# Performance work log

Measured on AMD Instinct MI355X. Metric: run time of the kernel, lower is better.

The kernel has to match this reference:

```python
import jax, jax.numpy as jnp
import numpy as np

N_USERS = 100_000
N_ITEMS = 50_000
N_EDGES = 2_000_000
D = 64
ALPHA = 0.5      # tanh-blend coefficient (alpha)
NORM_2 = -1.0    # exponent on back-aggregation degree norm (args.norm_2)


def setup_inputs() -> dict:
    key = jax.random.key(0)
    k1, k2, k3, k4, k5 = jax.random.split(key, 5)
    return {
        "h_user": jax.random.normal(k1, (N_USERS, D), jnp.float32) * 0.1,
        "pretrained_feature": jax.random.normal(k2, (N_ITEMS, D), jnp.float32),
        "edge_w": jax.random.normal(k3, (N_ITEMS, 1), jnp.float32),
        "src_idx": jax.random.randint(k4, (N_EDGES,), 0, N_USERS, dtype=jnp.int32),
        "dst_idx": jax.random.randint(k5, (N_EDGES,), 0, N_ITEMS, dtype=jnp.int32),
    }


def reference(h_user, pretrained_feature, edge_w, src_idx, dst_idx):
    # HGCNLayer.forward: bidirectional copy_src+sum aggregation with degree norm,
    # tanh prompt blend and node-softmax edge weighting.
    ones = jnp.ones((N_EDGES,), h_user.dtype)

    # forward pass user -> item: rst[d] = sum_{(s,d) in E} h_user[s]
    rst = jax.ops.segment_sum(h_user[src_idx], dst_idx, num_segments=N_ITEMS)  # [N_ITEMS, D]
    deg_dst = jnp.clip(jax.ops.segment_sum(ones, dst_idx, num_segments=N_ITEMS), 1.0)

    # alpha * tanh prompt blend
    rst = rst + ALPHA * jnp.tanh(pretrained_feature)
    # edge-prompt softmax scaling (softmax over nodes; see notes)
    rst = jax.nn.softmax(edge_w, axis=0) * rst
    # in-degree^-1 normalization
    rst = rst / deg_dst[:, None]

    # backward pass item -> user: bsrc[s] = sum_{(s,d) in E} rst[d]
    bsrc = jax.ops.segment_sum(rst[dst_idx], src_idx, num_segments=N_USERS)  # [N_USERS, D]
    deg_src = jnp.clip(jax.ops.segment_sum(ones, src_idx, num_segments=N_USERS), 1.0)
    bsrc = bsrc * jnp.power(deg_src, NORM_2)[:, None]
    return bsrc
```

## Files before the change

### kernel.cpp

```cpp
#include <hip/hip_runtime.h>
#include <hip/hip_bf16.h>
#include <math.h>

#define N_USERS 100000
#define N_ITEMS 50000
#define N_EDGES 2000000
#define D 64

#define FB_BINS 98
#define BB_BINS 196
#define NBINS   (FB_BINS + BB_BINS)
#define CHUNK   2048
#define NCHUNK  ((N_EDGES + CHUNK - 1) / CHUNK)
#define FOFF_F_N (FB_BINS * 512 + 1)
#define FOFF_B_N (BB_BINS * 512 + 1)
#define TOTSLOT  (2 * N_EDGES)
#define FWD_WGS (N_ITEMS / 16)
#define BWD_WGS ((N_USERS + 15) / 16)

__device__ __forceinline__ float blo(unsigned u) {
    union { unsigned i; float f; } c; c.i = u << 16; return c.f;
}
__device__ __forceinline__ float bhi(unsigned u) {
    union { unsigned i; float f; } c; c.i = u & 0xFFFF0000u; return c.f;
}
__device__ __forceinline__ unsigned bpack(float x, float y) {
    __hip_bfloat16 a = __float2bfloat16(x), b = __float2bfloat16(y);
    unsigned short ua = *reinterpret_cast<unsigned short*>(&a);
    unsigned short ub = *reinterpret_cast<unsigned short*>(&b);
    return (unsigned)ua | ((unsigned)ub << 16);
}

__global__ __launch_bounds__(256) void prep_kernel(
    const float2* __restrict__ hin, unsigned* __restrict__ hu16,
    const int* __restrict__ src, const int* __restrict__ dst,
    int* __restrict__ gh) {
    __shared__ int h[NBINS];
    for (int i = threadIdx.x; i < NBINS; i += 256) h[i] = 0;
    __syncthreads();
    int stride = gridDim.x * blockDim.x;
    int t0 = blockIdx.x * blockDim.x + threadIdx.x;
    for (int i = t0; i < N_USERS * 32; i += stride) {
        float2 v = hin[i];
        hu16[i] = bpack(v.x, v.y);
    }
    for (int e = t0; e < N_EDGES; e += stride) {
        atomicAdd(&h[dst[e] >> 9], 1);
        atomicAdd(&h[FB_BINS + (src[e] >> 9)], 1);
    }
    __syncthreads();
    for (int i = threadIdx.x; i < NBINS; i += 256) {
        int v = h[i];
        if (v) atomicAdd(&gh[i], v);
    }
}

__global__ void scan_soft_kernel(const int* __restrict__ in, int* __restrict__ out,
                                 int* __restrict__ cur,
                                 const float* __restrict__ w, float* __restrict__ stats) {
    __shared__ float redf[16];
    __shared__ int wsum[16];
    int tid = threadIdx.x, lane = tid & 63, wid = tid >> 6;

    if (blockIdx.x == 0) {
        int idx0 = tid * 4;
        int v[4]; int tot = 0;
#pragma unroll
        for (int e = 0; e < 4; e++) {
            int i = idx0 + e;
            v[e] = (i < NBINS) ? in[i] : 0;
            tot += v[e];
        }
        int incl = tot;
#pragma unroll
        for (int off = 1; off < 64; off <<= 1) {
            int t = __shfl_up(incl, off);
            if (lane >= off) incl += t;
        }
        if (lane == 63) wsum[wid] = incl;
        __syncthreads();
        if (wid == 0 && lane < 16) {
            int t = wsum[lane];
            int sc = t;
#pragma unroll
            for (int off = 1; off < 16; off <<= 1) {
                int u = __shfl_up(sc, off);
                if (lane >= off) sc += u;
            }
            wsum[lane] = sc - t;
        }
        __syncthreads();
        int excl = wsum[wid] + incl - tot;
#pragma unroll
        for (int e = 0; e < 4; e++) {
            int i = idx0 + e;
            if (i < NBINS) { out[i] = excl; cur[i] = excl; }
            if (i == NBINS) out[i] = excl;
            excl += v[e];
        }
        if (tid == 1023) out[NBINS] = excl;
        return;
    }

    float m = -INFINITY;
    for (int i = tid; i < N_ITEMS; i += 1024) m = fmaxf(m, w[i]);
#pragma unroll
    for (int off = 32; off; off >>= 1) m = fmaxf(m, __shfl_xor(m, off));
    if (lane == 0) redf[wid] = m;
    __syncthreads();
    if (tid == 0) {
        float t = redf[0];
        for (int k = 1; k < 16; k++) t = fmaxf(t, redf[k]);
        redf[0] = t;
    }
    __syncthreads();
    m = redf[0];
    __syncthreads();

    float s = 0.f;
    for (int i = tid; i < N_ITEMS; i += 1024) s += expf(w[i] - m);
#pragma unroll
    for (int off = 32; off; off >>= 1) s += __shfl_xor(s, off);
    if (lane == 0) redf[wid] = s;
    __syncthreads();
    if (tid == 0) {
        float t = 0.f;
        for (int k = 0; k < 16; k++) t += redf[k];
        stats[0] = m;
        stats[1] = t;
    }
}

__global__ __launch_bounds__(256) void binfill_kernel(
    const int* __restrict__ src, const int* __restrict__ dst,
    int* __restrict__ gcur, unsigned* __restrict__ stage) {
    __shared__ int cnt[NBINS];
    __shared__ int gbase[NBINS];
    __shared__ int lcur[NBINS];
    int c = blockIdx.x;
    int base = c * CHUNK;
    int nEdge = N_EDGES - base; if (nEdge > CHUNK) nEdge = CHUNK;

    for (int t = threadIdx.x; t < NBINS; t += 256) { cnt[t] = 0; lcur[t] = 0; }
    __syncthreads();

    int es[8], ed[8];
#pragma unroll
    for (int j = 0; j < 8; j++) {
        int k = j * 256 + threadIdx.x;
        if (k < nEdge) {
            es[j] = src[base + k];
            ed[j] = dst[base + k];
            atomicAdd(&cnt[ed[j] >> 9], 1);
            atomicAdd(&cnt[FB_BINS + (es[j] >> 9)], 1);
        } else {
            es[j] = -1;
        }
    }
    __syncthreads();
    for (int t = threadIdx.x; t < NBINS; t += 256) {
        int cv = cnt[t];
        gbase[t] = cv ? atomicAdd(&gcur[t], cv) : 0;
    }
    __syncthreads();
#pragma unroll
    for (int j = 0; j < 8; j++) {
        if (es[j] >= 0) {
            int s = es[j], d = ed[j];
            int bf = d >> 9;
            int p = atomicAdd(&lcur[bf], 1);
            stage[gbase[bf] + p] = (unsigned)s | ((unsigned)(d & 511) << 17);
            int bb = FB_BINS + (s >> 9);
            int q = atomicAdd(&lcur[bb], 1);
            stage[gbase[bb] + q] = (unsigned)d | ((unsigned)(s & 511) << 16);
        }
    }
}

__global__ __launch_bounds__(512) void redist3_kernel(
    const unsigned* __restrict__ stage, const int* __restrict__ binoff,
    unsigned* __restrict__ stage2, int* __restrict__ foff_f, int* __restrict__ foff_b) {
    __shared__ int cnt[512];
    __shared__ int wsum[8];
    int wg = blockIdx.x, t = threadIdx.x, lane = t & 63, wv = t >> 6;

    if (wg < FB_BINS) {
        int B = wg;
        int beg = binoff[B], end = binoff[B + 1];
        cnt[t] = 0;
        __syncthreads();
        for (int k = beg + t; k < end; k += 512) {
            unsigned e = stage[k];
            atomicAdd(&cnt[(e >> 17) & 511], 1);
        }
        __syncthreads();
        int v = cnt[t];
        int incl = v;
#pragma unroll
        for (int off = 1; off < 64; off <<= 1) {
            int u = __shfl_up(incl, off);
            if (lane >= off) incl += u;
        }
        if (lane == 63) wsum[wv] = incl;
        __syncthreads();
        if (t == 0) {
            int run = 0;
#pragma unroll
            for (int k2 = 0; k2 < 8; k2++) { int x = wsum[k2]; wsum[k2] = run; run += x; }
        }
        __syncthreads();
        int base = beg + wsum[wv] + incl - v;
        foff_f[(B << 9) | t] = base;
        cnt[t] = base;
        if (B == FB_BINS - 1 && t == 0) foff_f[FB_BINS * 512] = end;
        __syncthreads();
        for (int k = beg + t; k < end; k += 512) {
            unsigned e = stage[k];
            int p = atomicAdd(&cnt[(e >> 17) & 511], 1);
            stage2[p] = e & 0x1FFFFu;
        }
    } else {
        for (int pass = 0; pass < 2; pass++) {
            int B = FB_BINS + ((wg - FB_BINS) << 1) + pass;
            int beg = binoff[B], end = binoff[B + 1];
            cnt[t] = 0;
            __syncthreads();
            for (int k = beg + t; k < end; k += 512) {
                unsigned e = stage[k];
                atomicAdd(&cnt[(e >> 16) & 511], 1);
            }
            __syncthreads();
            int v = cnt[t];
            int incl = v;
#pragma unroll
            for (int off = 1; off < 64; off <<= 1) {
                int u = __shfl_up(incl, off);
                if (lane >= off) incl += u;
            }
            if (lane == 63) wsum[wv] = incl;
            __syncthreads();
            if (t == 0) {
                int run = 0;
#pragma unroll
                for (int k2 = 0; k2 < 8; k2++) { int x = wsum[k2]; wsum[k2] = run; run += x; }
            }
            __syncthreads();
            int base = beg + wsum[wv] + incl - v;
            foff_b[((B - FB_BINS) << 9) | t] = base;
            cnt[t] = base;
            if (B == NBINS - 1 && t == 0) foff_b[BB_BINS * 512] = end;
            __syncthreads();
            for (int k = beg + t; k < end; k += 512) {
                unsigned e = stage[k];
                int p = atomicAdd(&cnt[(e >> 16) & 511], 1);
                stage2[p] = e & 0xFFFFu;
            }
            __syncthreads();
        }
    }
}

__global__ __launch_bounds__(256) void fwd_gather_kernel(
    const unsigned* __restrict__ hu16, const float* __restrict__ pf,
    const float* __restrict__ edge_w, const unsigned* __restrict__ stage2,
    const int* __restrict__ foff_f, const float* __restrict__ stats,
    unsigned* __restrict__ rst16) {
    int tid = threadIdx.x, lane = tid & 63, wv = tid >> 6;
    int q = lane & 31, half = lane >> 5;
    float m = stats[0], ssum = stats[1];
    const float2* PF2 = (const float2*)pf;
    int i0 = blockIdx.x * 16;

    for (int il = wv; il < 16; il += 4) {
        int i = i0 + il;
        if (i >= N_ITEMS) break;
        int a = foff_f[i], b = foff_f[i + 1];
        float ax = 0.f, ay = 0.f;
        int k = a;
        for (; k + 16 <= b; k += 16) {
            int s0 = (int)__builtin_nontemporal_load(&stage2[k + half]);
            int s1 = (int)__builtin_nontemporal_load(&stage2[k + 2 + half]);
            int s2 = (int)__builtin_nontemporal_load(&stage2[k + 4 + half]);
            int s3 = (int)__builtin_nontemporal_load(&stage2[k + 6 + half]);
            int s4 = (int)__builtin_nontemporal_load(&stage2[k + 8 + half]);
            int s5 = (int)__builtin_nontemporal_load(&stage2[k + 10 + half]);
            int s6 = (int)__builtin_nontemporal_load(&stage2[k + 12 + half]);
            int s7 = (int)__builtin_nontemporal_load(&stage2[k + 14 + half]);
            unsigned u0 = hu16[(s0 << 5) + q];
            unsigned u1 = hu16[(s1 << 5) + q];
            unsigned u2 = hu16[(s2 << 5) + q];
            unsigned u3 = hu16[(s3 << 5) + q];
            unsigned u4 = hu16[(s4 << 5) + q];
            unsigned u5 = hu16[(s5 << 5) + q];
            unsigned u6 = hu16[(s6 << 5) + q];
            unsigned u7 = hu16[(s7 << 5) + q];
            ax += ((blo(u0) + blo(u1)) + (blo(u2) + blo(u3)))
                + ((blo(u4) + blo(u5)) + (blo(u6) + blo(u7)));
            ay += ((bhi(u0) + bhi(u1)) + (bhi(u2) + bhi(u3)))
                + ((bhi(u4) + bhi(u5)) + (bhi(u6) + bhi(u7)));
        }
        if (k + 8 <= b) {
            int s0 = (int)__builtin_nontemporal_load(&stage2[k + half]);
            int s1 = (int)__builtin_nontemporal_load(&stage2[k + 2 + half]);
            int s2 = (int)__builtin_nontemporal_load(&stage2[k + 4 + half]);
            int s3 = (int)__builtin_nontemporal_load(&stage2[k + 6 + half]);
            unsigned u0 = hu16[(s0 << 5) + q];
            unsigned u1 = hu16[(s1 << 5) + q];
            unsigned u2 = hu16[(s2 << 5) + q];
            unsigned u3 = hu16[(s3 << 5) + q];
            ax += (blo(u0) + blo(u1)) + (blo(u2) + blo(u3));
            ay += (bhi(u0) + bhi(u1)) + (bhi(u2) + bhi(u3));
            k += 8;
        }
        for (; k + 2 <= b; k += 2) {
            unsigned u = hu16[((int)__builtin_nontemporal_load(&stage2[k + half]) << 5) + q];
            ax += blo(u); ay += bhi(u);
        }
        if (k < b && half == 0) {
            unsigned u = hu16[((int)__builtin_nontemporal_load(&stage2[k]) << 5) + q];
            ax += blo(u); ay += bhi(u);
        }
        ax += __shfl_xor(ax, 32);
        ay += __shfl_xor(ay, 32);
        if (half == 0) {
            float deg = (float)(b - a);
            if (deg < 1.f) deg = 1.f;
            float sc = expf(edge_w[i] - m) / (ssum * deg);
            float2 pv = PF2[(size_t)i * 32 + q];
            float vx = (ax + 0.5f * tanhf(pv.x)) * sc;
            float vy = (ay + 0.5f * tanhf(pv.y)) * sc;
            rst16[(size_t)i * 32 + q] = bpack(vx, vy);
        }
    }
}

__global__ __launch_bounds__(256) void bwd_gather_kernel(
    const unsigned* __restrict__ rst16, const unsigned* __restrict__ stage2,
    const int* __restrict__ foff_b, float* __restrict__ out) {
    int tid = threadIdx.x, lane = tid & 63, wv = tid >> 6;
    int q = lane & 31, half = lane >> 5;
    float2* OUT2 = (float2*)out;
    int u0i = blockIdx.x * 16;

    for (int il = wv; il < 16; il += 4) {
        int u = u0i + il;
        if (u >= N_USERS) break;
        int a = foff_b[u], b = foff_b[u + 1];
        float ax = 0.f, ay = 0.f;
        int k = a;
        for (; k + 16 <= b; k += 16) {
            int d0 = (int)__builtin_nontemporal_load(&stage2[k + half]);
            int d1 = (int)__builtin_nontemporal_load(&stage2[k + 2 + half]);
            int d2 = (int)__builtin_nontemporal_load(&stage2[k + 4 + half]);
            int d3 = (int)__builtin_nontemporal_load(&stage2[k + 6 + half]);
            int d4 = (int)__builtin_nontemporal_load(&stage2[k + 8 + half]);
            int d5 = (int)__builtin_nontemporal_load(&stage2[k + 10 + half]);
            int d6 = (int)__builtin_nontemporal_load(&stage2[k + 12 + half]);
            int d7 = (int)__builtin_nontemporal_load(&stage2[k + 14 + half]);
            unsigned u0 = rst16[(d0 << 5) + q];
            unsigned u1 = rst16[(d1 << 5) + q];
            unsigned u2 = rst16[(d2 << 5) + q];
            unsigned u3 = rst16[(d3 << 5) + q];
            unsigned u4 = rst16[(d4 << 5) + q];
            unsigned u5 = rst16[(d5 << 5) + q];
            unsigned u6 = rst16[(d6 << 5) + q];
            unsigned u7 = rst16[(d7 << 5) + q];
            ax += ((blo(u0) + blo(u1)) + (blo(u2) + blo(u3)))
                + ((blo(u4) + blo(u5)) + (blo(u6) + blo(u7)));
            ay += ((bhi(u0) + bhi(u1)) + (bhi(u2) + bhi(u3)))
                + ((bhi(u4) + bhi(u5)) + (bhi(u6) + bhi(u7)));
        }
        if (k + 8 <= b) {
            int d0 = (int)__builtin_nontemporal_load(&stage2[k + half]);
            int d1 = (int)__builtin_nontemporal_load(&stage2[k + 2 + half]);
            int d2 = (int)__builtin_nontemporal_load(&stage2[k + 4 + half]);
            int d3 = (int)__builtin_nontemporal_load(&stage2[k + 6 + half]);
            unsigned u0 = rst16[(d0 << 5) + q];
            unsigned u1 = rst16[(d1 << 5) + q];
            unsigned u2 = rst16[(d2 << 5) + q];
            unsigned u3 = rst16[(d3 << 5) + q];
            ax += (blo(u0) + blo(u1)) + (blo(u2) + blo(u3));
            ay += (bhi(u0) + bhi(u1)) + (bhi(u2) + bhi(u3));
            k += 8;
        }
        for (; k + 2 <= b; k += 2) {
            unsigned e = rst16[((int)__builtin_nontemporal_load(&stage2[k + half]) << 5) + q];
            ax += blo(e); ay += bhi(e);
        }
        if (k < b && half == 0) {
            unsigned e = rst16[((int)__builtin_nontemporal_load(&stage2[k]) << 5) + q];
            ax += blo(e); ay += bhi(e);
        }
        ax += __shfl_xor(ax, 32);
        ay += __shfl_xor(ay, 32);
        if (half == 0) {
            float deg = (float)(b - a);
            if (deg < 1.f) deg = 1.f;
            OUT2[(size_t)u * 32 + q] = make_float2(ax / deg, ay / deg);
        }
    }
}

extern "C" void kernel_launch(void* const* d_in, const int* in_sizes, int n_in,
                              void* d_out, int out_size, void* d_ws, size_t ws_size,
                              hipStream_t stream) {
    const float* h_user = (const float*)d_in[0];
    const float* pf     = (const float*)d_in[1];
    const float* edge_w = (const float*)d_in[2];
    const int*   src    = (const int*)d_in[3];
    const int*   dst    = (const int*)d_in[4];
    float* out = (float*)d_out;

    char* p = (char*)d_ws;
    int* gh      = (int*)p;     p += sizeof(int) * NBINS;
    int* binoff  = (int*)p;     p += sizeof(int) * (NBINS + 1);
    int* gcur    = (int*)p;     p += sizeof(int) * NBINS;
    int* foff_f  = (int*)p;     p += sizeof(int) * FOFF_F_N;
    int* foff_b  = (int*)p;     p += sizeof(int) * FOFF_B_N;
    float* stats = (float*)p;   p += 4 * sizeof(float);
    unsigned* stage  = (unsigned*)p; p += sizeof(unsigned) * (size_t)TOTSLOT;
    unsigned* stage2 = (unsigned*)p; p += sizeof(unsigned) * (size_t)TOTSLOT;
    unsigned* hu16   = (unsigned*)p; p += sizeof(unsigned) * (size_t)N_USERS * 32;
    unsigned* rst16  = (unsigned*)p; p += sizeof(unsigned) * (size_t)N_ITEMS * 32;

    hipMemsetAsync(gh, 0, sizeof(int) * NBINS, stream);

    prep_kernel<<<1024, 256, 0, stream>>>((const float2*)h_user, hu16, src, dst, gh);
    scan_soft_kernel<<<2, 1024, 0, stream>>>(gh, binoff, gcur, edge_w, stats);
    binfill_kernel<<<NCHUNK, 256, 0, stream>>>(src, dst, gcur, stage);
    redist3_kernel<<<196, 512, 0, stream>>>(stage, binoff, stage2, foff_f, foff_b);
    fwd_gather_kernel<<<FWD_WGS, 256, 0, stream>>>(hu16, pf, edge_w, stage2, foff_f, stats, rst16);
    bwd_gather_kernel<<<BWD_WGS, 256, 0, stream>>>(rst16, stage2, foff_b, out);
}
```

Measured before the change: 344.3 us.

## Shard forward gather by source range to improve cache locality

```diff
diff --git a/kernel.cpp b/kernel.cpp
--- a/kernel.cpp
+++ b/kernel.cpp
@@ -10,13 +10,14 @@
 #define FB_BINS 98
 #define BB_BINS 196
 #define NBINS   (FB_BINS + BB_BINS)
-#define CHUNK   2048
+#define CHUNK   4096
 #define NCHUNK  ((N_EDGES + CHUNK - 1) / CHUNK)
-#define FOFF_F_N (FB_BINS * 512 + 1)
+#define FOFF_F_N (FB_BINS * 1024 + 1)
 #define FOFF_B_N (BB_BINS * 512 + 1)
 #define TOTSLOT  (2 * N_EDGES)
 #define FWD_WGS (N_ITEMS / 16)
 #define BWD_WGS ((N_USERS + 15) / 16)
+#define SHARD_SPLIT 50000
 
 __device__ __forceinline__ float blo(unsigned u) {
     union { unsigned i; float f; } c; c.i = u << 16; return c.f;
@@ -29,6 +30,55 @@
     unsigned short ua = *reinterpret_cast<unsigned short*>(&a);
     unsigned short ub = *reinterpret_cast<unsigned short*>(&b);
     return (unsigned)ua | ((unsigned)ub << 16);
+}
+
+__device__ __forceinline__ void gather_run(
+    const unsigned* __restrict__ tbl, const unsigned* __restrict__ stage2,
+    int a, int b, int q, int half, float& ax, float& ay) {
+    int k = a;
+    for (; k + 16 <= b; k += 16) {
+        int s0 = (int)__builtin_nontemporal_load(&stage2[k + half]);
+        int s1 = (int)__builtin_nontemporal_load(&stage2[k + 2 + half]);
+        int s2 = (int)__builtin_nontemporal_load(&stage2[k + 4 + half]);
+        int s3 = (int)__builtin_nontemporal_load(&stage2[k + 6 + half]);
+        int s4 = (int)__builtin_nontemporal_load(&stage2[k + 8 + half]);
+        int s5 = (int)__builtin_nontemporal_load(&stage2[k + 10 + half]);
+        int s6 = (int)__builtin_nontemporal_load(&stage2[k + 12 + half]);
+        int s7 = (int)__builtin_nontemporal_load(&stage2[k + 14 + half]);
+        unsigned u0 = tbl[(s0 << 5) + q];
+        unsigned u1 = tbl[(s1 << 5) + q];
+        unsigned u2 = tbl[(s2 << 5) + q];
+        unsigned u3 = tbl[(s3 << 5) + q];
+        unsigned u4 = tbl[(s4 << 5) + q];
+        unsigned u5 = tbl[(s5 << 5) + q];
+        unsigned u6 = tbl[(s6 << 5) + q];
+        unsigned u7 = tbl[(s7 << 5) + q];
+        ax += ((blo(u0) + blo(u1)) + (blo(u2) + blo(u3)))
+            + ((blo(u4) + blo(u5)) + (blo(u6) + blo(u7)));
+        ay += ((bhi(u0) + bhi(u1)) + (bhi(u2) + bhi(u3)))
+            + ((bhi(u4) + bhi(u5)) + (bhi(u6) + bhi(u7)));
+    }
+    if (k + 8 <= b) {
+        int s0 = (int)__builtin_nontemporal_load(&stage2[k + half]);
+        int s1 = (int)__builtin_nontemporal_load(&stage2[k + 2 + half]);
+        int s2 = (int)__builtin_nontemporal_load(&stage2[k + 4 + half]);
+        int s3 = (int)__builtin_nontemporal_load(&stage2[k + 6 + half]);
+        unsigned u0 = tbl[(s0 << 5) + q];
+        unsigned u1 = tbl[(s1 << 5) + q];
+        unsigned u2 = tbl[(s2 << 5) + q];
+        unsigned u3 = tbl[(s3 << 5) + q];
+        ax += (blo(u0) + blo(u1)) + (blo(u2) + blo(u3));
+        ay += (bhi(u0) + bhi(u1)) + (bhi(u2) + bhi(u3));
+        k += 8;
+    }
+    for (; k + 2 <= b; k += 2) {
+        unsigned u = tbl[((int)__builtin_nontemporal_load(&stage2[k + half]) << 5) + q];
+        ax += blo(u); ay += bhi(u);
+    }
+    if (k < b && half == 0) {
+        unsigned u = tbl[((int)__builtin_nontemporal_load(&stage2[k]) << 5) + q];
+        ax += blo(u); ay += bhi(u);
+    }
 }
 
 __global__ __launch_bounds__(256) void prep_kernel(
@@ -98,7 +148,6 @@
             if (i == NBINS) out[i] = excl;
             excl += v[e];
         }
-        if (tid == 1023) out[NBINS] = excl;
         return;
     }
 
@@ -144,9 +193,9 @@
     for (int t = threadIdx.x; t < NBINS; t += 256) { cnt[t] = 0; lcur[t] = 0; }
     __syncthreads();
 
-    int es[8], ed[8];
-#pragma unroll
-    for (int j = 0; j < 8; j++) {
+    int es[16], ed[16];
+#pragma unroll
+    for (int j = 0; j < 16; j++) {
         int k = j * 256 + threadIdx.x;
         if (k < nEdge) {
             es[j] = src[base + k];
@@ -164,7 +213,7 @@
     }
     __syncthreads();
 #pragma unroll
-    for (int j = 0; j < 8; j++) {
+    for (int j = 0; j < 16; j++) {
         if (es[j] >= 0) {
             int s = es[j], d = ed[j];
             int bf = d >> 9;
@@ -180,21 +229,24 @@
 __global__ __launch_bounds__(512) void redist3_kernel(
     const unsigned* __restrict__ stage, const int* __restrict__ binoff,
     unsigned* __restrict__ stage2, int* __restrict__ foff_f, int* __restrict__ foff_b) {
-    __shared__ int cnt[512];
+    __shared__ int cnt[1024];
     __shared__ int wsum[8];
     int wg = blockIdx.x, t = threadIdx.x, lane = t & 63, wv = t >> 6;
 
     if (wg < FB_BINS) {
         int B = wg;
         int beg = binoff[B], end = binoff[B + 1];
-        cnt[t] = 0;
+        cnt[t] = 0; cnt[t + 512] = 0;
         __syncthreads();
         for (int k = beg + t; k < end; k += 512) {
             unsigned e = stage[k];
-            atomicAdd(&cnt[(e >> 17) & 511], 1);
-        }
-        __syncthreads();
-        int v = cnt[t];
+            int key = (int)((e >> 17) & 511) << 1;
+            key |= ((e & 0x1FFFFu) >= SHARD_SPLIT) ? 1 : 0;
+            atomicAdd(&cnt[key], 1);
+        }
+        __syncthreads();
+        int c0 = cnt[t << 1], c1 = cnt[(t << 1) | 1];
+        int v = c0 + c1;
         int incl = v;
 #pragma unroll
         for (int off = 1; off < 64; off <<= 1) {
@@ -210,13 +262,18 @@
         }
         __syncthreads();
         int base = beg + wsum[wv] + incl - v;
-        foff_f[(B << 9) | t] = base;
-        cnt[t] = base;
-        if (B == FB_BINS - 1 && t == 0) foff_f[FB_BINS * 512] = end;
+        int slot = (B << 10) | (t << 1);
+        foff_f[slot] = base;
+        foff_f[slot | 1] = base + c0;
+        cnt[t << 1] = base;
+        cnt[(t << 1) | 1] = base + c0;
+        if (B == FB_BINS - 1 && t == 0) foff_f[FB_BINS * 1024] = end;
         __syncthreads();
         for (int k = beg + t; k < end; k += 512) {
             unsigned e = stage[k];
-            int p = atomicAdd(&cnt[(e >> 17) & 511], 1);
+            int key = (int)((e >> 17) & 511) << 1;
+            key |= ((e & 0x1FFFFu) >= SHARD_SPLIT) ? 1 : 0;
+            int p = atomicAdd(&cnt[key], 1);
             stage2[p] = e & 0x1FFFFu;
         }
     } else {
@@ -260,11 +317,34 @@
     }
 }
 
-__global__ __launch_bounds__(256) void fwd_gather_kernel(
+__global__ __launch_bounds__(256) void fwd_s0_kernel(
+    const unsigned* __restrict__ hu16, const unsigned* __restrict__ stage2,
+    const int* __restrict__ foff_f, float* __restrict__ pacc) {
+    int tid = threadIdx.x, lane = tid & 63, wv = tid >> 6;
+    int q = lane & 31, half = lane >> 5;
+    int i0 = blockIdx.x * 16;
+
+    for (int il = wv; il < 16; il += 4) {
+        int i = i0 + il;
+        if (i >= N_ITEMS) break;
+        int a = foff_f[i << 1], b = foff_f[(i << 1) | 1];
+        float ax = 0.f, ay = 0.f;
+        gather_run(hu16, stage2, a, b, q, half, ax, ay);
+        ax += __shfl_xor(ax, 32);
+        ay += __shfl_xor(ay, 32);
+        if (half == 0) {
+            size_t off = ((size_t)i * 32 + q) * 2;
+            __builtin_nontemporal_store(ax, &pacc[off]);
+            __builtin_nontemporal_store(ay, &pacc[off + 1]);
+        }
+    }
+}
+
+__global__ __launch_bounds__(256) void fwd_s1_kernel(
     const unsigned* __restrict__ hu16, const float* __restrict__ pf,
     const float* __restrict__ edge_w, const unsigned* __restrict__ stage2,
     const int* __restrict__ foff_f, const float* __restrict__ stats,
-    unsigned* __restrict__ rst16) {
+    const float* __restrict__ pacc, unsigned* __restrict__ rst16) {
     int tid = threadIdx.x, lane = tid & 63, wv = tid >> 6;
     int q = lane & 31, half = lane >> 5;
     float m = stats[0], ssum = stats[1];
@@ -274,56 +354,18 @@
     for (int il = wv; il < 16; il += 4) {
         int i = i0 + il;
         if (i >= N_ITEMS) break;
-        int a = foff_f[i], b = foff_f[i + 1];
+        int a = foff_f[(i << 1) | 1], b = foff_f[(i << 1) + 2];
+        int a0 = foff_f[i << 1];
         float ax = 0.f, ay = 0.f;
-        int k = a;
-        for (; k + 16 <= b; k += 16) {
-            int s0 = (int)__builtin_nontemporal_load(&stage2[k + half]);
-            int s1 = (int)__builtin_nontemporal_load(&stage2[k + 2 + half]);
-            int s2 = (int)__builtin_nontemporal_load(&stage2[k + 4 + half]);
-            int s3 = (int)__builtin_nontemporal_load(&stage2[k + 6 + half]);
-            int s4 = (int)__builtin_nontemporal_load(&stage2[k + 8 + half]);
-            int s5 = (int)__builtin_nontemporal_load(&stage2[k + 10 + half]);
-            int s6 = (int)__builtin_nontemporal_load(&stage2[k + 12 + half]);
-            int s7 = (int)__builtin_nontemporal_load(&stage2[k + 14 + half]);
-            unsigned u0 = hu16[(s0 << 5) + q];
-            unsigned u1 = hu16[(s1 << 5) + q];
-            unsigned u2 = hu16[(s2 << 5) + q];
-            unsigned u3 = hu16[(s3 << 5) + q];
-            unsigned u4 = hu16[(s4 << 5) + q];
-            unsigned u5 = hu16[(s5 << 5) + q];
-            unsigned u6 = hu16[(s6 << 5) + q];
-            unsigned u7 = hu16[(s7 << 5) + q];
-            ax += ((blo(u0) + blo(u1)) + (blo(u2) + blo(u3)))
-                + ((blo(u4) + blo(u5)) + (blo(u6) + blo(u7)));
-            ay += ((bhi(u0) + bhi(u1)) + (bhi(u2) + bhi(u3)))
-                + ((bhi(u4) + bhi(u5)) + (bhi(u6) + bhi(u7)));
-        }
-        if (k + 8 <= b) {
-            int s0 = (int)__builtin_nontemporal_load(&stage2[k + half]);
-            int s1 = (int)__builtin_nontemporal_load(&stage2[k + 2 + half]);
-            int s2 = (int)__builtin_nontemporal_load(&stage2[k + 4 + half]);
-            int s3 = (int)__builtin_nontemporal_load(&stage2[k + 6 + half]);
-            unsigned u0 = hu16[(s0 << 5) + q];
-            unsigned u1 = hu16[(s1 << 5) + q];
-            unsigned u2 = hu16[(s2 << 5) + q];
-            unsigned u3 = hu16[(s3 << 5) + q];
-            ax += (blo(u0) + blo(u1)) + (blo(u2) + blo(u3));
-            ay += (bhi(u0) + bhi(u1)) + (bhi(u2) + bhi(u3));
-            k += 8;
-        }
-        for (; k + 2 <= b; k += 2) {
-            unsigned u = hu16[((int)__builtin_nontemporal_load(&stage2[k + half]) << 5) + q];
-            ax += blo(u); ay += bhi(u);
-        }
-        if (k < b && half == 0) {
-            unsigned u = hu16[((int)__builtin_nontemporal_load(&stage2[k]) << 5) + q];
-            ax += blo(u); ay += bhi(u);
-        }
+        gather_run(hu16, stage2, a, b, q, half, ax, ay);
         ax += __shfl_xor(ax, 32);
         ay += __shfl_xor(ay, 32);
         if (half == 0) {
-            float deg = (float)(b - a);
+            size_t off = ((size_t)i * 32 + q) * 2;
+            float px = __builtin_nontemporal_load(&pacc[off]);
+            float py = __builtin_nontemporal_load(&pacc[off + 1]);
+            ax += px; ay += py;
+            float deg = (float)(b - a0);
             if (deg < 1.f) deg = 1.f;
             float sc = expf(edge_w[i] - m) / (ssum * deg);
             float2 pv = PF2[(size_t)i * 32 + q];
@@ -347,50 +389,7 @@
         if (u >= N_USERS) break;
         int a = foff_b[u], b = foff_b[u + 1];
         float ax = 0.f, ay = 0.f;
-        int k = a;
-        for (; k + 16 <= b; k += 16) {
-            int d0 = (int)__builtin_nontemporal_load(&stage2[k + half]);
-            int d1 = (int)__builtin_nontemporal_load(&stage2[k + 2 + half]);
-            int d2 = (int)__builtin_nontemporal_load(&stage2[k + 4 + half]);
-            int d3 = (int)__builtin_nontemporal_load(&stage2[k + 6 + half]);
-            int d4 = (int)__builtin_nontemporal_load(&stage2[k + 8 + half]);
-            int d5 = (int)__builtin_nontemporal_load(&stage2[k + 10 + half]);
-            int d6 = (int)__builtin_nontemporal_load(&stage2[k + 12 + half]);
-            int d7 = (int)__builtin_nontemporal_load(&stage2[k + 14 + half]);
-            unsigned u0 = rst16[(d0 << 5) + q];
-            unsigned u1 = rst16[(d1 << 5) + q];
-            unsigned u2 = rst16[(d2 << 5) + q];
-            unsigned u3 = rst16[(d3 << 5) + q];
-            unsigned u4 = rst16[(d4 << 5) + q];
-            unsigned u5 = rst16[(d5 << 5) + q];
-            unsigned u6 = rst16[(d6 << 5) + q];
-            unsigned u7 = rst16[(d7 << 5) + q];
-            ax += ((blo(u0) + blo(u1)) + (blo(u2) + blo(u3)))
-                + ((blo(u4) + blo(u5)) + (blo(u6) + blo(u7)));
-            ay += ((bhi(u0) + bhi(u1)) + (bhi(u2) + bhi(u3)))
-                + ((bhi(u4) + bhi(u5)) + (bhi(u6) + bhi(u7)));
-        }
-        if (k + 8 <= b) {
-            int d0 = (int)__builtin_nontemporal_load(&stage2[k + half]);
-            int d1 = (int)__builtin_nontemporal_load(&stage2[k + 2 + half]);
-            int d2 = (int)__builtin_nontemporal_load(&stage2[k + 4 + half]);
-            int d3 = (int)__builtin_nontemporal_load(&stage2[k + 6 + half]);
-            unsigned u0 = rst16[(d0 << 5) + q];
-            unsigned u1 = rst16[(d1 << 5) + q];
-            unsigned u2 = rst16[(d2 << 5) + q];
-            unsigned u3 = rst16[(d3 << 5) + q];
-            ax += (blo(u0) + blo(u1)) + (blo(u2) + blo(u3));
-            ay += (bhi(u0) + bhi(u1)) + (bhi(u2) + bhi(u3));
-            k += 8;
-        }
-        for (; k + 2 <= b; k += 2) {
-            unsigned e = rst16[((int)__builtin_nontemporal_load(&stage2[k + half]) << 5) + q];
-            ax += blo(e); ay += bhi(e);
-        }
-        if (k < b && half == 0) {
-            unsigned e = rst16[((int)__builtin_nontemporal_load(&stage2[k]) << 5) + q];
-            ax += blo(e); ay += bhi(e);
-        }
+        gather_run(rst16, stage2, a, b, q, half, ax, ay);
         ax += __shfl_xor(ax, 32);
         ay += __shfl_xor(ay, 32);
         if (half == 0) {
@@ -422,6 +421,7 @@
     unsigned* stage2 = (unsigned*)p; p += sizeof(unsigned) * (size_t)TOTSLOT;
     unsigned* hu16   = (unsigned*)p; p += sizeof(unsigned) * (size_t)N_USERS * 32;
     unsigned* rst16  = (unsigned*)p; p += sizeof(unsigned) * (size_t)N_ITEMS * 32;
+    float* pacc      = (float*)p;    p += sizeof(float) * (size_t)N_ITEMS * 64;
 
     hipMemsetAsync(gh, 0, sizeof(int) * NBINS, stream);
 
@@ -429,6 +429,7 @@
     scan_soft_kernel<<<2, 1024, 0, stream>>>(gh, binoff, gcur, edge_w, stats);
     binfill_kernel<<<NCHUNK, 256, 0, stream>>>(src, dst, gcur, stage);
     redist3_kernel<<<196, 512, 0, stream>>>(stage, binoff, stage2, foff_f, foff_b);
-    fwd_gather_kernel<<<FWD_WGS, 256, 0, stream>>>(hu16, pf, edge_w, stage2, foff_f, stats, rst16);
+    fwd_s0_kernel<<<FWD_WGS, 256, 0, stream>>>(hu16, stage2, foff_f, pacc);
+    fwd_s1_kernel<<<FWD_WGS, 256, 0, stream>>>(hu16, pf, edge_w, stage2, foff_f, stats, pacc, rst16);
     bwd_gather_kernel<<<BWD_WGS, 256, 0, stream>>>(rst16, stage2, foff_b, out);
 }
```

New measurement: 346.4 us. Within noise of the previous version (+0.6%).
